# Performance work log

Measured on AMD Instinct MI355X. Metric: run time of the kernel, lower is better.

The kernel has to match this reference:

```python
import jax, jax.numpy as jnp
import numpy as np

DIM = 512
HEADS = 8
HEAD_DIM = DIM // HEADS
FF = 2048
WIN = 128
TIME_DIM = 512
B, N = 8, 8192
EPS = 1e-5
NEG = -1e9


def setup_inputs() -> dict:
    key = jax.random.key(0)
    ks = jax.random.split(key, 16)
    def lin(k, fan_in, fan_out):
        bound = 1.0 / np.sqrt(fan_in)
        kw, kb = jax.random.split(k)
        W = jax.random.uniform(kw, (fan_in, fan_out), jnp.float32, -bound, bound)
        b = jax.random.uniform(kb, (fan_out,), jnp.float32, -bound, bound)
        return W, b
    qkv_w, qkv_b = lin(ks[0], DIM, 3 * DIM)
    proj_w, proj_b = lin(ks[1], DIM, DIM)
    mlp_w1, mlp_b1 = lin(ks[2], DIM, FF)
    mlp_w2, mlp_b2 = lin(ks[3], FF, DIM)
    time_w, time_b = lin(ks[4], TIME_DIM, 2 * DIM)
    return {
        "x": jax.random.normal(ks[5], (B, N, DIM), jnp.float32),
        "t_emb": jax.random.normal(ks[6], (B, TIME_DIM), jnp.float32),
        "ln1_g": jnp.ones((DIM,), jnp.float32), "ln1_b": jnp.zeros((DIM,), jnp.float32),
        "qkv_w": qkv_w, "qkv_b": qkv_b,
        "proj_w": proj_w, "proj_b": proj_b,
        "ln2_g": jnp.ones((DIM,), jnp.float32), "ln2_b": jnp.zeros((DIM,), jnp.float32),
        "mlp_w1": mlp_w1, "mlp_b1": mlp_b1,
        "mlp_w2": mlp_w2, "mlp_b2": mlp_b2,
        "time_w": time_w, "time_b": time_b,
    }


def _layernorm(x, g, b):
    mu = jnp.mean(x, -1, keepdims=True)
    var = jnp.mean(jnp.square(x - mu), -1, keepdims=True)
    return (x - mu) * jax.lax.rsqrt(var + EPS) * g + b


def _local_attention(q, k, v, w):
    # q,k,v: [B, h, N, d]; each w-window attends to [prev|cur|next] windows.
    Bh_B, h, n, d = q.shape
    nW = n // w
    qw = q.reshape(Bh_B * h, nW, w, d)
    kw = k.reshape(Bh_B * h, nW, w, d)
    vw = v.reshape(Bh_B * h, nW, w, d)
    pad = lambda t: jnp.pad(t, ((0, 0), (1, 1), (0, 0), (0, 0)))
    kp, vp = pad(kw), pad(vw)
    # context: [Bh, nW, 3w, d]
    kc = jnp.concatenate([kp[:, :-2], kp[:, 1:-1], kp[:, 2:]], axis=2)
    vc = jnp.concatenate([vp[:, :-2], vp[:, 1:-1], vp[:, 2:]], axis=2)
    wv = jnp.pad(jnp.ones((nW,), bool), (1, 1))  # window validity
    valid = jnp.concatenate([
        jnp.repeat(wv[:-2, None], w, 1),
        jnp.repeat(wv[1:-1, None], w, 1),
        jnp.repeat(wv[2:, None], w, 1)], axis=1)  # [nW, 3w]
    sim = jnp.einsum('bnid,bnjd->bnij', qw, kc) * (d ** -0.5)
    sim = jnp.where(valid[None, :, None, :], sim, NEG)
    attn = jax.nn.softmax(sim, axis=-1)
    out = jnp.einsum('bnij,bnjd->bnid', attn, vc)
    return out.reshape(Bh_B, h, n, d)


def reference(x, t_emb, ln1_g, ln1_b, qkv_w, qkv_b, proj_w, proj_b,
              ln2_g, ln2_b, mlp_w1, mlp_b1, mlp_w2, mlp_b2, time_w, time_b):
    Bq, n, c = x.shape
    ss = jax.nn.silu(t_emb) @ time_w + time_b  # [B, 2C]
    scale, shift = ss[:, :c], ss[:, c:]
    x_norm = _layernorm(x, ln1_g, ln1_b) * (1.0 + scale[:, None, :]) + shift[:, None, :]
    qkv = (x_norm @ qkv_w + qkv_b).reshape(Bq, n, 3, HEADS, HEAD_DIM)
    qkv = jnp.transpose(qkv, (2, 0, 3, 1, 4))  # [3, B, h, N, d]
    q, k, v = qkv[0], qkv[1], qkv[2]
    attn_out = _local_attention(q, k, v, WIN)  # [B, h, N, d]
    attn_out = jnp.transpose(attn_out, (0, 2, 1, 3)).reshape(Bq, n, c)
    x = x + (attn_out @ proj_w + proj_b)
    h2 = _layernorm(x, ln2_g, ln2_b)
    mlp = jax.nn.gelu(h2 @ mlp_w1 + mlp_b1, approximate=False) @ mlp_w2 + mlp_b2
    return x + mlp
```

## Files before the change

kernel.cpp:

```cpp
#include <hip/hip_runtime.h>
#include <cstdint>
#include <cstddef>

#define DIM   512
#define HEADS 8
#define HD    64
#define FF    2048
#define WINSZ 128
#define BB    8
#define NN    8192
#define NW    (NN / WINSZ)
#define MROWS (BB * NN)
#define QS    ((size_t)BB * HEADS * NN * HD)

typedef __attribute__((ext_vector_type(8))) _Float16 half8;
typedef __attribute__((ext_vector_type(4))) float floatx4;

__device__ __forceinline__ floatx4 mfma16(half8 a, half8 b, floatx4 c) {
    return __builtin_amdgcn_mfma_f32_16x16x32_f16(a, b, c, 0, 0, 0);
}

__device__ __forceinline__ void gload_lds16(const void* g, void* l) {
    __builtin_amdgcn_global_load_lds(
        (const __attribute__((address_space(1))) void*)g,
        (__attribute__((address_space(3))) void*)l, 16, 0, 0);
}

__device__ __forceinline__ float qmax16(float v) {
    v = fmaxf(v, __shfl_xor(v, 1));
    v = fmaxf(v, __shfl_xor(v, 2));
    v = fmaxf(v, __shfl_xor(v, 4));
    v = fmaxf(v, __shfl_xor(v, 8));
    return v;
}
__device__ __forceinline__ float qsum16(float v) {
    v += __shfl_xor(v, 1);
    v += __shfl_xor(v, 2);
    v += __shfl_xor(v, 4);
    v += __shfl_xor(v, 8);
    return v;
}

__device__ __forceinline__ float gelu_f(float x) {
    const float y = 1.5957691216f * (x + 0.044715f * x * x * x);
    const float t = 1.0f - 2.0f / (__expf(y) + 1.0f);
    return 0.5f * x * (1.0f + t);
}

__global__ __launch_bounds__(128)
void time_ss_kernel(const float* __restrict__ t_emb, const float* __restrict__ tw,
                    const float* __restrict__ tb, float* __restrict__ ss) {
    __shared__ float st[512];
    const int b = blockIdx.x;
    for (int i = threadIdx.x; i < 512; i += 128) {
        float v = t_emb[b * 512 + i];
        st[i] = v / (1.0f + expf(-v));
    }
    __syncthreads();
    const int j = blockIdx.y * 128 + threadIdx.x;
    float acc = tb[j];
    for (int i = 0; i < 512; ++i) acc += st[i] * tw[i * 1024 + j];
    ss[b * 1024 + j] = acc;
}

__global__ __launch_bounds__(256)
void wcast_kernel(const float* __restrict__ w, _Float16* __restrict__ wt, int K, int N) {
    __shared__ float t[32][33];
    const int kb = blockIdx.x * 32, nb = blockIdx.y * 32;
    const int tx = threadIdx.x & 31, ty = threadIdx.x >> 5;
#pragma unroll
    for (int i = 0; i < 32; i += 8)
        t[ty + i][tx] = w[(size_t)(kb + ty + i) * N + nb + tx];
    __syncthreads();
#pragma unroll
    for (int i = 0; i < 32; i += 8)
        wt[(size_t)(nb + ty + i) * K + kb + tx] = (_Float16)t[tx][ty + i];
}

template <bool MOD>
__global__ __launch_bounds__(256)
void ln_kernel(const float* __restrict__ x, const float* __restrict__ g,
               const float* __restrict__ bv, const float* __restrict__ ss,
               _Float16* __restrict__ out) {
    const int row  = blockIdx.x * 4 + (threadIdx.x >> 6);
    const int lane = threadIdx.x & 63;
    const float* xr = x + (size_t)row * DIM;
    const float4 v0 = *(const float4*)(xr + lane * 4);
    const float4 v1 = *(const float4*)(xr + 256 + lane * 4);
    float s  = v0.x + v0.y + v0.z + v0.w + v1.x + v1.y + v1.z + v1.w;
    float s2 = v0.x * v0.x + v0.y * v0.y + v0.z * v0.z + v0.w * v0.w +
               v1.x * v1.x + v1.y * v1.y + v1.z * v1.z + v1.w * v1.w;
#pragma unroll
    for (int m = 1; m < 64; m <<= 1) {
        s  += __shfl_xor(s, m);
        s2 += __shfl_xor(s2, m);
    }
    const float mean = s * (1.0f / 512.0f);
    const float var  = s2 * (1.0f / 512.0f) - mean * mean;
    const float rstd = rsqrtf(var + 1e-5f);
    const int b = row >> 13;
    const float vv[8] = {v0.x, v0.y, v0.z, v0.w, v1.x, v1.y, v1.z, v1.w};
    union { _Float16 h[4]; unsigned long long u; } pk;
#pragma unroll
    for (int half = 0; half < 2; ++half) {
        const int c0 = half * 256 + lane * 4;
#pragma unroll
        for (int i = 0; i < 4; ++i) {
            const int c = c0 + i;
            float y = (vv[half * 4 + i] - mean) * rstd * g[c] + bv[c];
            if (MOD) y = y * (1.0f + ss[b * 1024 + c]) + ss[b * 1024 + 512 + c];
            pk.h[i] = (_Float16)y;
        }
        *(unsigned long long*)(out + (size_t)row * DIM + c0) = pk.u;
    }
}

template <int EPI>
__global__ __launch_bounds__(256)
void gemm_bt(const _Float16* __restrict__ A, const _Float16* __restrict__ BT,
             const float* __restrict__ bias, int K, int N,
             const float* __restrict__ resid, float* __restrict__ outf,
             _Float16* __restrict__ outh) {
    __shared__ _Float16 lA[128 * 32];
    __shared__ _Float16 lB[128 * 32];
    const int tid  = threadIdx.x;
    const int wv   = tid >> 6;
    const int lane = tid & 63;
    const int ln   = lane & 15;
    const int qd   = lane >> 4;
    const int wm   = (wv >> 1) * 64;
    const int wn   = (wv & 1) * 64;
    const int m0   = blockIdx.y * 128;
    const int n0   = blockIdx.x * 128;

    floatx4 acc[4][4];
#pragma unroll
    for (int i = 0; i < 4; ++i)
#pragma unroll
        for (int j = 0; j < 4; ++j) acc[i][j] = (floatx4){0.f, 0.f, 0.f, 0.f};

    for (int kt = 0; kt < K; kt += 32) {
        __syncthreads();
#pragma unroll
        for (int i = 0; i < 2; ++i) {
            const int c    = tid + i * 256;
            const int row  = c >> 2;
            const int kc   = (c & 3) * 8;
            const int base = (wv * 64 + i * 256) * 8;
            gload_lds16(A + (size_t)(m0 + row) * K + kt + kc, &lA[base]);
            gload_lds16(BT + (size_t)(n0 + row) * K + kt + kc, &lB[base]);
        }
        __syncthreads();
        half8 af[4], bf[4];
#pragma unroll
        for (int mi = 0; mi < 4; ++mi)
            af[mi] = *(const half8*)&lA[(wm + mi * 16 + ln) * 32 + qd * 8];
#pragma unroll
        for (int ni = 0; ni < 4; ++ni)
            bf[ni] = *(const half8*)&lB[(wn + ni * 16 + ln) * 32 + qd * 8];
#pragma unroll
        for (int mi = 0; mi < 4; ++mi)
#pragma unroll
            for (int ni = 0; ni < 4; ++ni)
                acc[mi][ni] = mfma16(af[mi], bf[ni], acc[mi][ni]);
    }

#pragma unroll
    for (int mi = 0; mi < 4; ++mi) {
#pragma unroll
        for (int ni = 0; ni < 4; ++ni) {
            const int col  = n0 + wn + ni * 16 + ln;
            const float bb = bias[col];
#pragma unroll
            for (int r = 0; r < 4; ++r) {
                const int row = m0 + wm + mi * 16 + qd * 4 + r;
                const float v = acc[mi][ni][r] + bb;
                if (EPI == 0) {
                    const int which = col >> 9, cc = col & 511;
                    const int b = row >> 13, t = row & 8191;
                    const int h = cc >> 6, d = cc & 63;
                    outh[(size_t)which * QS +
                         ((size_t)(b * HEADS + h) * NN + t) * HD + d] = (_Float16)v;
                } else if (EPI == 1 || EPI == 3) {
                    const size_t idx = (size_t)row * N + col;
                    outf[idx] = resid[idx] + v;
                } else {
                    outh[(size_t)row * N + col] = (_Float16)gelu_f(v);
                }
            }
        }
    }
}

__global__ __launch_bounds__(256)
void attn_kernel(const _Float16* __restrict__ qkv, _Float16* __restrict__ attn) {
    const int w  = blockIdx.x;
    const int bh = blockIdx.y;
    const int tid  = threadIdx.x;
    const int wv   = tid >> 6;
    const int lane = tid & 63;
    const int ln   = lane & 15;
    const int qd   = lane >> 4;

    __shared__ _Float16 vt[64 * 136];
    __shared__ _Float16 pl[4 * 32 * 136];

    const _Float16* qbuf = qkv;
    const _Float16* kbuf = qkv + QS;
    const _Float16* vbuf = qkv + 2 * QS;
    const size_t bhbase = (size_t)bh * NN * HD;

    half8 qf[2][2];
    const _Float16* qsrc = qbuf + bhbase + (size_t)(w * WINSZ + wv * 32) * HD;
#pragma unroll
    for (int mt = 0; mt < 2; ++mt)
#pragma unroll
        for (int ks = 0; ks < 2; ++ks)
            qf[mt][ks] = *(const half8*)(qsrc + (mt * 16 + ln) * HD + ks * 32 + qd * 8);

    float mrun[2][4], lrun[2][4];
    floatx4 oacc[2][4];
#pragma unroll
    for (int mt = 0; mt < 2; ++mt)
#pragma unroll
        for (int r = 0; r < 4; ++r) { mrun[mt][r] = -3.0e38f; lrun[mt][r] = 0.f; }
#pragma unroll
    for (int mt = 0; mt < 2; ++mt)
#pragma unroll
        for (int dt = 0; dt < 4; ++dt) oacc[mt][dt] = (floatx4){0.f, 0.f, 0.f, 0.f};

    for (int c = 0; c < 3; ++c) {
        const int kvw = w + c - 1;
        if (kvw < 0 || kvw >= NW) continue;
        __syncthreads();
        const _Float16* vsrc = vbuf + bhbase + (size_t)kvw * WINSZ * HD;
#pragma unroll
        for (int j = 0; j < 4; ++j) {
            const int cc = tid + j * 256;
            const int s = cc >> 3, d0 = (cc & 7) * 8;
            half8 vvv = *(const half8*)(vsrc + cc * 8);
#pragma unroll
            for (int e = 0; e < 8; ++e) vt[(d0 + e) * 136 + s] = vvv[e];
        }
        __syncthreads();

        const _Float16* ksrc = kbuf + bhbase + (size_t)kvw * WINSZ * HD;
        floatx4 sacc[2][8];
#pragma unroll
        for (int nt = 0; nt < 8; ++nt) {
            half8 b0 = *(const half8*)(ksrc + (nt * 16 + ln) * HD + qd * 8);
            half8 b1 = *(const half8*)(ksrc + (nt * 16 + ln) * HD + 32 + qd * 8);
#pragma unroll
            for (int mt = 0; mt < 2; ++mt) {
                floatx4 t = mfma16(qf[mt][0], b0, (floatx4){0.f, 0.f, 0.f, 0.f});
                sacc[mt][nt] = mfma16(qf[mt][1], b1, t);
            }
        }

        _Float16* pw = pl + wv * 32 * 136;
#pragma unroll
        for (int mt = 0; mt < 2; ++mt) {
#pragma unroll
            for (int r = 0; r < 4; ++r) {
                float mx = -3.0e38f;
#pragma unroll
                for (int nt = 0; nt < 8; ++nt)
                    mx = fmaxf(mx, sacc[mt][nt][r] * 0.125f);
                mx = qmax16(mx);
                const float mnew  = fmaxf(mrun[mt][r], mx);
                const float alpha = __expf(mrun[mt][r] - mnew);
                float rs = 0.f;
#pragma unroll
                for (int nt = 0; nt < 8; ++nt) {
                    const float pv = __expf(sacc[mt][nt][r] * 0.125f - mnew);
                    rs += pv;
                    pw[(mt * 16 + qd * 4 + r) * 136 + nt * 16 + ln] = (_Float16)pv;
                }
                rs = qsum16(rs);
                lrun[mt][r] = lrun[mt][r] * alpha + rs;
                mrun[mt][r] = mnew;
#pragma unroll
                for (int dt = 0; dt < 4; ++dt) oacc[mt][dt][r] *= alpha;
            }
        }

#pragma unroll
        for (int kt = 0; kt < 4; ++kt) {
            half8 pf0 = *(const half8*)(pw + ln * 136 + kt * 32 + qd * 8);
            half8 pf1 = *(const half8*)(pw + (16 + ln) * 136 + kt * 32 + qd * 8);
#pragma unroll
            for (int dt = 0; dt < 4; ++dt) {
                half8 vf = *(const half8*)&vt[(dt * 16 + ln) * 136 + kt * 32 + qd * 8];
                oacc[0][dt] = mfma16(pf0, vf, oacc[0][dt]);
                oacc[1][dt] = mfma16(pf1, vf, oacc[1][dt]);
            }
        }
    }

    const int b = bh >> 3, h = bh & 7;
#pragma unroll
    for (int mt = 0; mt < 2; ++mt) {
#pragma unroll
        for (int dt = 0; dt < 4; ++dt) {
#pragma unroll
            for (int r = 0; r < 4; ++r) {
                const int trow = w * WINSZ + wv * 32 + mt * 16 + qd * 4 + r;
                const int col  = h * HD + dt * 16 + ln;
                attn[((size_t)b * NN + trow) * DIM + col] =
                    (_Float16)(oacc[mt][dt][r] / lrun[mt][r]);
            }
        }
    }
}

extern "C" void kernel_launch(void* const* d_in, const int* in_sizes, int n_in,
                              void* d_out, int out_size, void* d_ws, size_t ws_size,
                              hipStream_t stream) {
    const float* x      = (const float*)d_in[0];
    const float* t_emb  = (const float*)d_in[1];
    const float* ln1_g  = (const float*)d_in[2];
    const float* ln1_b  = (const float*)d_in[3];
    const float* qkv_w  = (const float*)d_in[4];
    const float* qkv_b  = (const float*)d_in[5];
    const float* proj_w = (const float*)d_in[6];
    const float* proj_b = (const float*)d_in[7];
    const float* ln2_g  = (const float*)d_in[8];
    const float* ln2_b  = (const float*)d_in[9];
    const float* mlp_w1 = (const float*)d_in[10];
    const float* mlp_b1 = (const float*)d_in[11];
    const float* mlp_w2 = (const float*)d_in[12];
    const float* mlp_b2 = (const float*)d_in[13];
    const float* time_w = (const float*)d_in[14];
    const float* time_b = (const float*)d_in[15];
    float* out = (float*)d_out;

    char* p = (char*)d_ws;
    auto alloc = [&](size_t bytes) {
        char* r = p;
        p += (bytes + 255) & ~(size_t)255;
        return r;
    };
    float*    ss   = (float*)alloc(8 * 1024 * 4);
    _Float16* wq   = (_Float16*)alloc((size_t)1536 * 512 * 2);
    _Float16* wp   = (_Float16*)alloc((size_t)512 * 512 * 2);
    _Float16* w1t  = (_Float16*)alloc((size_t)2048 * 512 * 2);
    _Float16* w2t  = (_Float16*)alloc((size_t)512 * 2048 * 2);
    _Float16* h2   = (_Float16*)alloc((size_t)MROWS * 512 * 2);
    float*    x1   = (float*)alloc((size_t)MROWS * 512 * 4);
    _Float16* regA = (_Float16*)alloc((size_t)MROWS * 512 * 2);
    _Float16* regB = (_Float16*)alloc((size_t)3 * MROWS * 512 * 2);
    _Float16* xn     = regA;
    _Float16* attn   = regA;
    _Float16* qkvb   = regB;
    _Float16* hidden = regA;
    (void)ws_size; (void)in_sizes; (void)n_in; (void)out_size;

    wcast_kernel<<<dim3(512 / 32, 1536 / 32), 256, 0, stream>>>(qkv_w, wq, 512, 1536);
    wcast_kernel<<<dim3(512 / 32, 512 / 32), 256, 0, stream>>>(proj_w, wp, 512, 512);
    wcast_kernel<<<dim3(512 / 32, 2048 / 32), 256, 0, stream>>>(mlp_w1, w1t, 512, 2048);
    wcast_kernel<<<dim3(2048 / 32, 512 / 32), 256, 0, stream>>>(mlp_w2, w2t, 2048, 512);
    time_ss_kernel<<<dim3(8, 8), 128, 0, stream>>>(t_emb, time_w, time_b, ss);
    ln_kernel<true><<<dim3(MROWS / 4), 256, 0, stream>>>(x, ln1_g, ln1_b, ss, xn);
    gemm_bt<0><<<dim3(1536 / 128, MROWS / 128), 256, 0, stream>>>(
        xn, wq, qkv_b, 512, 1536, nullptr, nullptr, qkvb);
    attn_kernel<<<dim3(NW, BB * HEADS), 256, 0, stream>>>(qkvb, attn);
    gemm_bt<1><<<dim3(512 / 128, MROWS / 128), 256, 0, stream>>>(
        attn, wp, proj_b, 512, 512, x, x1, nullptr);
    ln_kernel<false><<<dim3(MROWS / 4), 256, 0, stream>>>(x1, ln2_g, ln2_b, nullptr, h2);
    gemm_bt<2><<<dim3(2048 / 128, MROWS / 128), 256, 0, stream>>>(
        h2, w1t, mlp_b1, 512, 2048, nullptr, nullptr, hidden);
    gemm_bt<3><<<dim3(512 / 128, MROWS / 128), 256, 0, stream>>>(
        hidden, w2t, mlp_b2, 2048, 512, x1, out, nullptr);
}
```

Baseline: 1.347 ms.

## Deepen GEMM K-tile with XOR-swizzled LDS, group tiles, store residual in fp16

The GEMM K step is doubled from 32 to 64, and the LDS layout gets an XOR swizzle so fragment reads avoid bank conflicts. Output tiles are remapped into groups of 8 M-rows per N column to improve L2 reuse. The intermediate residual x1 is now stored as fp16 instead of fp32, and a new fp16-input LayerNorm kernel reads it, which cuts memory traffic. The cost is lower precision on the residual path, plus twice the shared memory per GEMM block.

```diff
diff --git a/kernel.cpp b/kernel.cpp
--- a/kernel.cpp
+++ b/kernel.cpp
@@ -77,7 +77,6 @@
         wt[(size_t)(nb + ty + i) * K + kb + tx] = (_Float16)t[tx][ty + i];
 }
 
-template <bool MOD>
 __global__ __launch_bounds__(256)
 void ln_kernel(const float* __restrict__ x, const float* __restrict__ g,
                const float* __restrict__ bv, const float* __restrict__ ss,
@@ -108,21 +107,52 @@
         for (int i = 0; i < 4; ++i) {
             const int c = c0 + i;
             float y = (vv[half * 4 + i] - mean) * rstd * g[c] + bv[c];
-            if (MOD) y = y * (1.0f + ss[b * 1024 + c]) + ss[b * 1024 + 512 + c];
+            y = y * (1.0f + ss[b * 1024 + c]) + ss[b * 1024 + 512 + c];
             pk.h[i] = (_Float16)y;
         }
         *(unsigned long long*)(out + (size_t)row * DIM + c0) = pk.u;
     }
+}
+
+__global__ __launch_bounds__(256)
+void ln_h_kernel(const _Float16* __restrict__ x, const float* __restrict__ g,
+                 const float* __restrict__ bv, _Float16* __restrict__ out) {
+    const int row  = blockIdx.x * 4 + (threadIdx.x >> 6);
+    const int lane = threadIdx.x & 63;
+    half8 v = *(const half8*)(x + (size_t)row * DIM + lane * 8);
+    float f[8];
+    float s = 0.f, s2 = 0.f;
+#pragma unroll
+    for (int i = 0; i < 8; ++i) {
+        f[i] = (float)v[i];
+        s += f[i];
+        s2 += f[i] * f[i];
+    }
+#pragma unroll
+    for (int m = 1; m < 64; m <<= 1) {
+        s  += __shfl_xor(s, m);
+        s2 += __shfl_xor(s2, m);
+    }
+    const float mean = s * (1.0f / 512.0f);
+    const float var  = s2 * (1.0f / 512.0f) - mean * mean;
+    const float rstd = rsqrtf(var + 1e-5f);
+    half8 o;
+#pragma unroll
+    for (int i = 0; i < 8; ++i) {
+        const int c = lane * 8 + i;
+        o[i] = (_Float16)((f[i] - mean) * rstd * g[c] + bv[c]);
+    }
+    *(half8*)(out + (size_t)row * DIM + lane * 8) = o;
 }
 
 template <int EPI>
 __global__ __launch_bounds__(256)
 void gemm_bt(const _Float16* __restrict__ A, const _Float16* __restrict__ BT,
              const float* __restrict__ bias, int K, int N,
-             const float* __restrict__ resid, float* __restrict__ outf,
-             _Float16* __restrict__ outh) {
-    __shared__ _Float16 lA[128 * 32];
-    __shared__ _Float16 lB[128 * 32];
+             const float* __restrict__ residf, const _Float16* __restrict__ residh,
+             float* __restrict__ outf, _Float16* __restrict__ outh) {
+    __shared__ _Float16 lA[128 * 64];
+    __shared__ _Float16 lB[128 * 64];
     const int tid  = threadIdx.x;
     const int wv   = tid >> 6;
     const int lane = tid & 63;
@@ -130,8 +160,13 @@
     const int qd   = lane >> 4;
     const int wm   = (wv >> 1) * 64;
     const int wn   = (wv & 1) * 64;
-    const int m0   = blockIdx.y * 128;
-    const int n0   = blockIdx.x * 128;
+
+    const int nbx = gridDim.x;
+    const int l   = blockIdx.y * nbx + blockIdx.x;
+    const int grp = l / (nbx * 8);
+    const int rem = l - grp * (nbx * 8);
+    const int m0  = (grp * 8 + (rem & 7)) * 128;
+    const int n0  = (rem >> 3) * 128;
 
     floatx4 acc[4][4];
 #pragma unroll
@@ -139,30 +174,37 @@
 #pragma unroll
         for (int j = 0; j < 4; ++j) acc[i][j] = (floatx4){0.f, 0.f, 0.f, 0.f};
 
-    for (int kt = 0; kt < K; kt += 32) {
+    for (int kt = 0; kt < K; kt += 64) {
         __syncthreads();
 #pragma unroll
-        for (int i = 0; i < 2; ++i) {
-            const int c    = tid + i * 256;
-            const int row  = c >> 2;
-            const int kc   = (c & 3) * 8;
+        for (int i = 0; i < 4; ++i) {
+            const int c   = tid + i * 256;
+            const int row = c >> 3;
+            const int src = ((c & 7) ^ (row & 7)) * 8;
             const int base = (wv * 64 + i * 256) * 8;
-            gload_lds16(A + (size_t)(m0 + row) * K + kt + kc, &lA[base]);
-            gload_lds16(BT + (size_t)(n0 + row) * K + kt + kc, &lB[base]);
+            gload_lds16(A + (size_t)(m0 + row) * K + kt + src, &lA[base]);
+            gload_lds16(BT + (size_t)(n0 + row) * K + kt + src, &lB[base]);
         }
         __syncthreads();
-        half8 af[4], bf[4];
-#pragma unroll
-        for (int mi = 0; mi < 4; ++mi)
-            af[mi] = *(const half8*)&lA[(wm + mi * 16 + ln) * 32 + qd * 8];
-#pragma unroll
-        for (int ni = 0; ni < 4; ++ni)
-            bf[ni] = *(const half8*)&lB[(wn + ni * 16 + ln) * 32 + qd * 8];
-#pragma unroll
-        for (int mi = 0; mi < 4; ++mi)
-#pragma unroll
-            for (int ni = 0; ni < 4; ++ni)
-                acc[mi][ni] = mfma16(af[mi], bf[ni], acc[mi][ni]);
+#pragma unroll
+        for (int ks = 0; ks < 2; ++ks) {
+            half8 af[4], bf[4];
+#pragma unroll
+            for (int mi = 0; mi < 4; ++mi) {
+                const int row = wm + mi * 16 + ln;
+                af[mi] = *(const half8*)&lA[row * 64 + (((ks * 4 + qd) ^ (row & 7)) << 3)];
+            }
+#pragma unroll
+            for (int ni = 0; ni < 4; ++ni) {
+                const int row = wn + ni * 16 + ln;
+                bf[ni] = *(const half8*)&lB[row * 64 + (((ks * 4 + qd) ^ (row & 7)) << 3)];
+            }
+#pragma unroll
+            for (int mi = 0; mi < 4; ++mi)
+#pragma unroll
+                for (int ni = 0; ni < 4; ++ni)
+                    acc[mi][ni] = mfma16(af[mi], bf[ni], acc[mi][ni]);
+        }
     }
 
 #pragma unroll
@@ -181,9 +223,12 @@
                     const int h = cc >> 6, d = cc & 63;
                     outh[(size_t)which * QS +
                          ((size_t)(b * HEADS + h) * NN + t) * HD + d] = (_Float16)v;
-                } else if (EPI == 1 || EPI == 3) {
+                } else if (EPI == 1) {
                     const size_t idx = (size_t)row * N + col;
-                    outf[idx] = resid[idx] + v;
+                    outh[idx] = (_Float16)(residf[idx] + v);
+                } else if (EPI == 3) {
+                    const size_t idx = (size_t)row * N + col;
+                    outf[idx] = (float)residh[idx] + v;
                 } else {
                     outh[(size_t)row * N + col] = (_Float16)gelu_f(v);
                 }
@@ -346,7 +391,7 @@
     _Float16* w1t  = (_Float16*)alloc((size_t)2048 * 512 * 2);
     _Float16* w2t  = (_Float16*)alloc((size_t)512 * 2048 * 2);
     _Float16* h2   = (_Float16*)alloc((size_t)MROWS * 512 * 2);
-    float*    x1   = (float*)alloc((size_t)MROWS * 512 * 4);
+    _Float16* x1h  = (_Float16*)alloc((size_t)MROWS * 512 * 2);
     _Float16* regA = (_Float16*)alloc((size_t)MROWS * 512 * 2);
     _Float16* regB = (_Float16*)alloc((size_t)3 * MROWS * 512 * 2);
     _Float16* xn     = regA;
@@ -360,15 +405,15 @@
     wcast_kernel<<<dim3(512 / 32, 2048 / 32), 256, 0, stream>>>(mlp_w1, w1t, 512, 2048);
     wcast_kernel<<<dim3(2048 / 32, 512 / 32), 256, 0, stream>>>(mlp_w2, w2t, 2048, 512);
     time_ss_kernel<<<dim3(8, 8), 128, 0, stream>>>(t_emb, time_w, time_b, ss);
-    ln_kernel<true><<<dim3(MROWS / 4), 256, 0, stream>>>(x, ln1_g, ln1_b, ss, xn);
+    ln_kernel<<<dim3(MROWS / 4), 256, 0, stream>>>(x, ln1_g, ln1_b, ss, xn);
     gemm_bt<0><<<dim3(1536 / 128, MROWS / 128), 256, 0, stream>>>(
-        xn, wq, qkv_b, 512, 1536, nullptr, nullptr, qkvb);
+        xn, wq, qkv_b, 512, 1536, nullptr, nullptr, nullptr, qkvb);
     attn_kernel<<<dim3(NW, BB * HEADS), 256, 0, stream>>>(qkvb, attn);
     gemm_bt<1><<<dim3(512 / 128, MROWS / 128), 256, 0, stream>>>(
-        attn, wp, proj_b, 512, 512, x, x1, nullptr);
-    ln_kernel<false><<<dim3(MROWS / 4), 256, 0, stream>>>(x1, ln2_g, ln2_b, nullptr, h2);
+        attn, wp, proj_b, 512, 512, x, nullptr, nullptr, x1h);
+    ln_h_kernel<<<dim3(MROWS / 4), 256, 0, stream>>>(x1h, ln2_g, ln2_b, h2);
     gemm_bt<2><<<dim3(2048 / 128, MROWS / 128), 256, 0, stream>>>(
-        h2, w1t, mlp_b1, 512, 2048, nullptr, nullptr, hidden);
+        h2, w1t, mlp_b1, 512, 2048, nullptr, nullptr, nullptr, hidden);
     gemm_bt<3><<<dim3(512 / 128, MROWS / 128), 256, 0, stream>>>(
-        hidden, w2t, mlp_b2, 2048, 512, x1, out, nullptr);
-}
+        hidden, w2t, mlp_b2, 2048, 512, nullptr, x1h, out, nullptr);
+}
```

After: 1.264 ms. -6.2%, faster.
